# Kernel tuning notes

Hardware: AMD Instinct MI355X
Metric: run time of the kernel (lower is better)

The kernel has to match this reference:

```python
import jax, jax.numpy as jnp
import numpy as np

INPUT_DIM, HIDDEN, OUT_DIM = 7, 64, 4


def _lstm_layer(x_seq, W_ih, W_hh, b_ih, b_hh):
    """Single LSTM layer, batch_first x_seq [B,T,D] -> [B,T,H]. PyTorch gate order i,f,g,o."""
    B = x_seq.shape[0]
    H = W_hh.shape[1]
    # Precompute input projection for all timesteps (hoist GEMM out of the scan).
    x_proj = jnp.einsum('btd,gd->btg', x_seq, W_ih) + b_ih + b_hh  # [B,T,4H]

    def step(carry, xt):
        h, c = carry
        gates = xt + h @ W_hh.T  # [B,4H]
        i, f, g, o = jnp.split(gates, 4, axis=-1)
        i = jax.nn.sigmoid(i)
        f = jax.nn.sigmoid(f)
        g = jnp.tanh(g)
        o = jax.nn.sigmoid(o)
        c = f * c + i * g
        h = o * jnp.tanh(c)
        return (h, c), h

    h0 = jnp.zeros((B, H), x_seq.dtype)
    c0 = jnp.zeros((B, H), x_seq.dtype)
    (_, _), hs = jax.lax.scan(step, (h0, c0), jnp.swapaxes(x_proj, 0, 1))  # hs [T,B,H]
    return jnp.swapaxes(hs, 0, 1)  # [B,T,H]


def setup_inputs() -> dict:
    key = jax.random.key(0)
    ks = jax.random.split(key, 12)
    s = 0.1  # init scale ~ 1/sqrt(hidden)
    x = jax.random.normal(ks[0], (4096, 512, INPUT_DIM), dtype=jnp.float32)
    W_ih0 = jax.random.normal(ks[1], (4 * HIDDEN, INPUT_DIM), dtype=jnp.float32) * s
    W_hh0 = jax.random.normal(ks[2], (4 * HIDDEN, HIDDEN), dtype=jnp.float32) * s
    b_ih0 = jax.random.normal(ks[3], (4 * HIDDEN,), dtype=jnp.float32) * s
    b_hh0 = jax.random.normal(ks[4], (4 * HIDDEN,), dtype=jnp.float32) * s
    W_ih1 = jax.random.normal(ks[5], (4 * HIDDEN, HIDDEN), dtype=jnp.float32) * s
    W_hh1 = jax.random.normal(ks[6], (4 * HIDDEN, HIDDEN), dtype=jnp.float32) * s
    b_ih1 = jax.random.normal(ks[7], (4 * HIDDEN,), dtype=jnp.float32) * s
    b_hh1 = jax.random.normal(ks[8], (4 * HIDDEN,), dtype=jnp.float32) * s
    W_fc = jax.random.normal(ks[9], (OUT_DIM, HIDDEN), dtype=jnp.float32) * s
    b_fc = jax.random.normal(ks[10], (OUT_DIM,), dtype=jnp.float32) * s
    return {"x": x, "W_ih0": W_ih0, "W_hh0": W_hh0, "b_ih0": b_ih0, "b_hh0": b_hh0,
            "W_ih1": W_ih1, "W_hh1": W_hh1, "b_ih1": b_ih1, "b_hh1": b_hh1,
            "W_fc": W_fc, "b_fc": b_fc}


def reference(x, W_ih0, W_hh0, b_ih0, b_hh0, W_ih1, W_hh1, b_ih1, b_hh1, W_fc, b_fc):
    h1 = _lstm_layer(x, W_ih0, W_hh0, b_ih0, b_hh0)   # [B,T,H]
    h2 = _lstm_layer(h1, W_ih1, W_hh1, b_ih1, b_hh1)  # [B,T,H]
    last = h2[:, -1, :]                               # [B,H]
    return last @ W_fc.T + b_fc                       # [B,4]
```

## Files before the change

kernel.cpp:

```cpp
#include <hip/hip_runtime.h>

#define T_SEQ 512
#define HID 64
#define MB 16
#define NTHREADS 1024
#define A1STR 104
#define A2STR 104

typedef __attribute__((ext_vector_type(8))) short short8;
typedef __attribute__((ext_vector_type(4))) float floatx4;

#define LOG2E 1.4426950408889634f

__device__ __forceinline__ short f2bf_rne(float v) {
  unsigned u = __float_as_uint(v);
  return (short)((u + 0x7FFFu + ((u >> 16) & 1u)) >> 16);
}
__device__ __forceinline__ float rcp_(float x) { return __builtin_amdgcn_rcpf(x); }
__device__ __forceinline__ float exp2_(float x) { return __builtin_amdgcn_exp2f(x); }

__device__ __forceinline__ unsigned cvt_pk_bf16(float lo, float hi) {
  unsigned r;
  asm("v_cvt_pk_bf16_f32 %0, %1, %2" : "=v"(r) : "v"(lo), "v"(hi));
  return r;
}

__device__ __forceinline__ float gate_h(const floatx4 p, float& c) {
  float A = exp2_(-p[0]);
  float F = exp2_(-p[1]);
  float G = exp2_(p[2]);
  float O = exp2_(-p[3]);
  float t1 = (1.f + A) * (G + 1.f);
  float t2 = 1.f + F;
  float num = c * t1 + (G - 1.f) * t2;
  c = num * rcp_(t1 * t2);
  float C = exp2_((2.f * LOG2E) * c);
  return (C - 1.f) * rcp_((1.f + O) * (C + 1.f));
}

__device__ __forceinline__ int uofp(int p) {
  return (p & ~7) + ((p & 7) >> 1) + ((p & 1) << 2);
}

__device__ __forceinline__ short w1elem(int k, int n, float wsc,
                                        const float* __restrict__ Wih0,
                                        const float* __restrict__ Whh0) {
  float v;
  if      (k < 64) { v = Whh0[n*64 + uofp(k)]; }
  else if (k < 71) { v = Wih0[n*7 + (k - 64)]; }
  else return (short)0;
  return f2bf_rne(v * wsc);
}
__device__ __forceinline__ short w2elem(int k, int n, float wsc,
                                        const float* __restrict__ Wih1,
                                        const float* __restrict__ Whh1) {
  float v;
  if (k < 64) { v = Wih1[n*64 + uofp(k)]; }
  else        { v = Whh1[n*64 + uofp(k - 64)]; }
  return f2bf_rne(v * wsc);
}

#define MFMA(A, B, C) __builtin_amdgcn_mfma_f32_16x16x32_bf16((A), (B), (C), 0, 0, 0)

__global__ __launch_bounds__(NTHREADS, 4) void lstm_fused(
    const float* __restrict__ x,
    const float* __restrict__ Wih0, const float* __restrict__ Whh0,
    const float* __restrict__ bih0, const float* __restrict__ bhh0,
    const float* __restrict__ Wih1, const float* __restrict__ Whh1,
    const float* __restrict__ bih1, const float* __restrict__ bhh1,
    const float* __restrict__ Wfc,  const float* __restrict__ bfc,
    float* __restrict__ out)
{
  __shared__ __align__(16) short A1[2][MB][A1STR];
  __shared__ __align__(16) short A2[2][MB][A2STR];
  __shared__ float h2f[MB][HID + 4];

  const int tid  = threadIdx.x;
  const int lane = tid & 63;
  const int wave = tid >> 6;
  const int wl   = wave & 7;
  const bool isL1 = wave < 8;
  const int l15  = lane & 15;
  const int quad = lane >> 4;
  const int quad8= quad * 8;
  const int g4   = l15 & 3;
  const int b0   = blockIdx.x * MB;
  const int u0   = wl*8 + quad;
  const int u1   = u0 + 4;
  const int hpos = wl*8 + 2*quad;
  const int n0   = g4*64 + (wl*8 + (l15 >> 2));
  const int n1   = n0 + 4;
  const float wsc = (g4 == 2) ? 2.f * LOG2E : LOG2E;

  for (int i = tid; i < 2*MB*A1STR/2; i += NTHREADS) ((unsigned*)A1)[i] = 0u;
  for (int i = tid; i < 2*MB*A2STR/2; i += NTHREADS) ((unsigned*)A2)[i] = 0u;
  __syncthreads();

  const float* bi_ = isL1 ? bih0 : bih1;
  const float* bh_ = isL1 ? bhh0 : bhh1;
  floatx4 bia, bib;
  #pragma unroll
  for (int g = 0; g < 4; ++g) {
    float ws = (g == 2) ? 2.f * LOG2E : LOG2E;
    bia[g] = (bi_[g*64 + u0] + bh_[g*64 + u0]) * ws;
    bib[g] = (bi_[g*64 + u1] + bh_[g*64 + u1]) * ws;
  }

  const int xd2  = lane & 31;
  const int xrow = 2*wl + (lane >> 5);
  const bool xact = isL1 && (xd2 < 4);
  const float* xbase = x + ((size_t)(b0 + xrow) * T_SEQ) * 7 + 2*xd2;
  float xc0 = 0.f, xc1 = 0.f;
  if (xact) {
    *(unsigned*)&A1[0][xrow][64 + 2*xd2] =
        cvt_pk_bf16(xbase[0], (xd2 < 3) ? xbase[1] : 0.f);
    xc0 = xbase[7];
    xc1 = (xd2 < 3) ? xbase[8] : 0.f;
  }

  short8 WA[4], WB[4];
  if (isL1) {
    #pragma unroll
    for (int ks = 0; ks < 3; ++ks) {
      short8 fa, fb;
      #pragma unroll
      for (int jj = 0; jj < 8; ++jj) {
        fa[jj] = w1elem(ks*32 + quad8 + jj, n0, wsc, Wih0, Whh0);
        fb[jj] = w1elem(ks*32 + quad8 + jj, n1, wsc, Wih0, Whh0);
      }
      WA[ks] = fa; WB[ks] = fb;
    }
  } else {
    #pragma unroll
    for (int ks = 0; ks < 4; ++ks) {
      short8 fa, fb;
      #pragma unroll
      for (int jj = 0; jj < 8; ++jj) {
        fa[jj] = w2elem(ks*32 + quad8 + jj, n0, wsc, Wih1, Whh1);
        fb[jj] = w2elem(ks*32 + quad8 + jj, n1, wsc, Wih1, Whh1);
      }
      WA[ks] = fa; WB[ks] = fb;
    }
  }
  __syncthreads();

  float ca = 0.f, cb = 0.f;

#define STEP_X(NXT, XT)                                                      \
    if (xact) {                                                              \
      *(unsigned*)&A1[NXT][xrow][64 + 2*xd2] = cvt_pk_bf16(xc0, xc1);        \
      xc0 = xbase[7 * (XT)];                                                 \
      xc1 = (xd2 < 3) ? xbase[7 * (XT) + 1] : 0.f;                           \
    }

#define STEP_FULL(CUR, NXT, IT)                                              \
  {                                                                          \
    if (isL1) {                                                              \
      int xt_ = (IT) + 2; if (xt_ > T_SEQ - 1) xt_ = T_SEQ - 1;              \
      STEP_X(NXT, xt_)                                                       \
      short8 hf0 = *(const short8*)&A1[CUR][l15][     quad8];                \
      short8 hf1 = *(const short8*)&A1[CUR][l15][32 + quad8];                \
      short8 hfx = *(const short8*)&A1[CUR][l15][64 + quad8];                \
      floatx4 pa = bia, pb = bib;                                            \
      pa = MFMA(WA[0], hf0, pa);  pb = MFMA(WB[0], hf0, pb);                 \
      pa = MFMA(WA[1], hf1, pa);  pb = MFMA(WB[1], hf1, pb);                 \
      pa = MFMA(WA[2], hfx, pa);  pb = MFMA(WB[2], hfx, pb);                 \
      float ha = gate_h(pa, ca);                                             \
      float hb = gate_h(pb, cb);                                             \
      *(unsigned*)&A1[NXT][l15][hpos] = cvt_pk_bf16(ha, hb);                 \
    } else {                                                                 \
      short8 hf0 = *(const short8*)&A1[CUR][l15][     quad8];                \
      short8 hf1 = *(const short8*)&A1[CUR][l15][32 + quad8];                \
      short8 h20 = *(const short8*)&A2[CUR][l15][     quad8];                \
      short8 h21 = *(const short8*)&A2[CUR][l15][32 + quad8];                \
      floatx4 pa = bia, pb = bib;                                            \
      pa = MFMA(WA[0], hf0, pa);  pb = MFMA(WB[0], hf0, pb);                 \
      pa = MFMA(WA[1], hf1, pa);  pb = MFMA(WB[1], hf1, pb);                 \
      pa = MFMA(WA[2], h20, pa);  pb = MFMA(WB[2], h20, pb);                 \
      pa = MFMA(WA[3], h21, pa);  pb = MFMA(WB[3], h21, pb);                 \
      float ha = gate_h(pa, ca);                                             \
      float hb = gate_h(pb, cb);                                             \
      *(unsigned*)&A2[NXT][l15][hpos] = cvt_pk_bf16(ha, hb);                 \
    }                                                                        \
    __syncthreads();                                                         \
  }

  {
    if (isL1) {
      STEP_X(1, 2)
      short8 hf0 = *(const short8*)&A1[0][l15][     quad8];
      short8 hf1 = *(const short8*)&A1[0][l15][32 + quad8];
      short8 hfx = *(const short8*)&A1[0][l15][64 + quad8];
      floatx4 pa = bia, pb = bib;
      pa = MFMA(WA[0], hf0, pa);  pb = MFMA(WB[0], hf0, pb);
      pa = MFMA(WA[1], hf1, pa);  pb = MFMA(WB[1], hf1, pb);
      pa = MFMA(WA[2], hfx, pa);  pb = MFMA(WB[2], hfx, pb);
      float ha = gate_h(pa, ca);
      float hb = gate_h(pb, cb);
      *(unsigned*)&A1[1][l15][hpos] = cvt_pk_bf16(ha, hb);
    }
    __syncthreads();
  }

  #pragma unroll 1
  for (int k = 0; k < 255; ++k) {
    STEP_FULL(1, 0, 2*k + 1)
    STEP_FULL(0, 1, 2*k + 2)
  }
  STEP_FULL(1, 0, 511)

  {
    if (!isL1) {
      short8 hf0 = *(const short8*)&A1[0][l15][     quad8];
      short8 hf1 = *(const short8*)&A1[0][l15][32 + quad8];
      short8 h20 = *(const short8*)&A2[0][l15][     quad8];
      short8 h21 = *(const short8*)&A2[0][l15][32 + quad8];
      floatx4 pa = bia, pb = bib;
      pa = MFMA(WA[0], hf0, pa);  pb = MFMA(WB[0], hf0, pb);
      pa = MFMA(WA[1], hf1, pa);  pb = MFMA(WB[1], hf1, pb);
      pa = MFMA(WA[2], h20, pa);  pb = MFMA(WB[2], h20, pb);
      pa = MFMA(WA[3], h21, pa);  pb = MFMA(WB[3], h21, pb);
      h2f[l15][u0] = gate_h(pa, ca);
      h2f[l15][u1] = gate_h(pb, cb);
    }
    __syncthreads();
  }

  if (tid < MB * 4) {
    int bbf = tid >> 2, o = tid & 3;
    float acc = bfc[o];
    #pragma unroll 8
    for (int kk = 0; kk < HID; ++kk) acc += h2f[bbf][kk] * Wfc[o*HID + kk];
    out[(size_t)(b0 + bbf) * 4 + o] = acc;
  }
}

extern "C" void kernel_launch(void* const* d_in, const int* in_sizes, int n_in,
                              void* d_out, int out_size, void* d_ws, size_t ws_size,
                              hipStream_t stream) {
  const float* x    = (const float*)d_in[0];
  const float* Wih0 = (const float*)d_in[1];
  const float* Whh0 = (const float*)d_in[2];
  const float* bih0 = (const float*)d_in[3];
  const float* bhh0 = (const float*)d_in[4];
  const float* Wih1 = (const float*)d_in[5];
  const float* Whh1 = (const float*)d_in[6];
  const float* bih1 = (const float*)d_in[7];
  const float* bhh1 = (const float*)d_in[8];
  const float* Wfc  = (const float*)d_in[9];
  const float* bfc  = (const float*)d_in[10];
  (void)d_ws; (void)ws_size; (void)n_in; (void)out_size;

  const int B = in_sizes[0] / (T_SEQ * 7);
  dim3 grid(B / MB);
  lstm_fused<<<grid, NTHREADS, 0, stream>>>(x, Wih0, Whh0, bih0, bhh0,
                                            Wih1, Whh1, bih1, bhh1, Wfc, bfc,
                                            (float*)d_out);
}
```

Before: 427.4 us.

## Halve block to 8 waves with four gate tiles per wave and lighter barrier

Each block now uses 512 threads instead of 1024: 4 waves per LSTM layer, each computing four 16-column MFMA tiles and four gate cells per lane instead of two, with the weight fragments held in registers. This cuts the number of waves that meet at each per-timestep barrier and lets more independent MFMA chains overlap within a wave. The __syncthreads is also replaced by a raw LDS waitcnt plus s_barrier. In exchange, register pressure per thread doubles, the occupancy hint drops to 2, and there is less parallelism across waves inside each step.

Measured after the change: 426.3 us. About the same (-0.3%).

```diff
diff --git a/kernel.cpp b/kernel.cpp
--- a/kernel.cpp
+++ b/kernel.cpp
@@ -3,7 +3,7 @@
 #define T_SEQ 512
 #define HID 64
 #define MB 16
-#define NTHREADS 1024
+#define NTHREADS 512
 #define A1STR 104
 #define A2STR 104
 
@@ -23,6 +23,12 @@
   unsigned r;
   asm("v_cvt_pk_bf16_f32 %0, %1, %2" : "=v"(r) : "v"(lo), "v"(hi));
   return r;
+}
+
+__device__ __forceinline__ void barrier_lds() {
+  asm volatile("s_waitcnt lgkmcnt(0)" ::: "memory");
+  __builtin_amdgcn_s_barrier();
+  asm volatile("" ::: "memory");
 }
 
 __device__ __forceinline__ float gate_h(const floatx4 p, float& c) {
@@ -62,7 +68,7 @@
 
 #define MFMA(A, B, C) __builtin_amdgcn_mfma_f32_16x16x32_bf16((A), (B), (C), 0, 0, 0)
 
-__global__ __launch_bounds__(NTHREADS, 4) void lstm_fused(
+__global__ __launch_bounds__(NTHREADS, 2) void lstm_fused(
     const float* __restrict__ x,
     const float* __restrict__ Wih0, const float* __restrict__ Whh0,
     const float* __restrict__ bih0, const float* __restrict__ bhh0,
@@ -78,18 +84,16 @@
   const int tid  = threadIdx.x;
   const int lane = tid & 63;
   const int wave = tid >> 6;
-  const int wl   = wave & 7;
-  const bool isL1 = wave < 8;
+  const int w0   = wave & 3;
+  const bool isL1 = wave < 4;
   const int l15  = lane & 15;
   const int quad = lane >> 4;
   const int quad8= quad * 8;
   const int g4   = l15 & 3;
   const int b0   = blockIdx.x * MB;
-  const int u0   = wl*8 + quad;
-  const int u1   = u0 + 4;
-  const int hpos = wl*8 + 2*quad;
-  const int n0   = g4*64 + (wl*8 + (l15 >> 2));
-  const int n1   = n0 + 4;
+  const int ub   = w0*16 + quad;
+  const int hp0  = w0*16 + 2*quad;
+  const int hp1  = hp0 + 8;
   const float wsc = (g4 == 2) ? 2.f * LOG2E : LOG2E;
 
   for (int i = tid; i < 2*MB*A1STR/2; i += NTHREADS) ((unsigned*)A1)[i] = 0u;
@@ -98,16 +102,18 @@
 
   const float* bi_ = isL1 ? bih0 : bih1;
   const float* bh_ = isL1 ? bhh0 : bhh1;
-  floatx4 bia, bib;
+  floatx4 bs0, bs1, bs2, bs3;
   #pragma unroll
   for (int g = 0; g < 4; ++g) {
     float ws = (g == 2) ? 2.f * LOG2E : LOG2E;
-    bia[g] = (bi_[g*64 + u0] + bh_[g*64 + u0]) * ws;
-    bib[g] = (bi_[g*64 + u1] + bh_[g*64 + u1]) * ws;
-  }
-
-  const int xd2  = lane & 31;
-  const int xrow = 2*wl + (lane >> 5);
+    bs0[g] = (bi_[g*64 + ub     ] + bh_[g*64 + ub     ]) * ws;
+    bs1[g] = (bi_[g*64 + ub + 4 ] + bh_[g*64 + ub + 4 ]) * ws;
+    bs2[g] = (bi_[g*64 + ub + 8 ] + bh_[g*64 + ub + 8 ]) * ws;
+    bs3[g] = (bi_[g*64 + ub + 12] + bh_[g*64 + ub + 12]) * ws;
+  }
+
+  const int xd2  = l15;
+  const int xrow = 4*w0 + quad;
   const bool xact = isL1 && (xd2 < 4);
   const float* xbase = x + ((size_t)(b0 + xrow) * T_SEQ) * 7 + 2*xd2;
   float xc0 = 0.f, xc1 = 0.f;
@@ -118,33 +124,31 @@
     xc1 = (xd2 < 3) ? xbase[8] : 0.f;
   }
 
-  short8 WA[4], WB[4];
+  short8 W0[4], W1[4], W2[4], W3[4];
+#define LOADW1(Wt, t)                                                        \
+  { int nt = g4*64 + w0*16 + 4*(t) + (l15 >> 2);                             \
+    _Pragma("unroll")                                                        \
+    for (int ks = 0; ks < 3; ++ks) { short8 f;                               \
+      _Pragma("unroll")                                                      \
+      for (int jj = 0; jj < 8; ++jj)                                         \
+        f[jj] = w1elem(ks*32 + quad8 + jj, nt, wsc, Wih0, Whh0);             \
+      Wt[ks] = f; } }
+#define LOADW2(Wt, t)                                                        \
+  { int nt = g4*64 + w0*16 + 4*(t) + (l15 >> 2);                             \
+    _Pragma("unroll")                                                        \
+    for (int ks = 0; ks < 4; ++ks) { short8 f;                               \
+      _Pragma("unroll")                                                      \
+      for (int jj = 0; jj < 8; ++jj)                                         \
+        f[jj] = w2elem(ks*32 + quad8 + jj, nt, wsc, Wih1, Whh1);             \
+      Wt[ks] = f; } }
   if (isL1) {
-    #pragma unroll
-    for (int ks = 0; ks < 3; ++ks) {
-      short8 fa, fb;
-      #pragma unroll
-      for (int jj = 0; jj < 8; ++jj) {
-        fa[jj] = w1elem(ks*32 + quad8 + jj, n0, wsc, Wih0, Whh0);
-        fb[jj] = w1elem(ks*32 + quad8 + jj, n1, wsc, Wih0, Whh0);
-      }
-      WA[ks] = fa; WB[ks] = fb;
-    }
+    LOADW1(W0, 0) LOADW1(W1, 1) LOADW1(W2, 2) LOADW1(W3, 3)
   } else {
-    #pragma unroll
-    for (int ks = 0; ks < 4; ++ks) {
-      short8 fa, fb;
-      #pragma unroll
-      for (int jj = 0; jj < 8; ++jj) {
-        fa[jj] = w2elem(ks*32 + quad8 + jj, n0, wsc, Wih1, Whh1);
-        fb[jj] = w2elem(ks*32 + quad8 + jj, n1, wsc, Wih1, Whh1);
-      }
-      WA[ks] = fa; WB[ks] = fb;
-    }
+    LOADW2(W0, 0) LOADW2(W1, 1) LOADW2(W2, 2) LOADW2(W3, 3)
   }
   __syncthreads();
 
-  float ca = 0.f, cb = 0.f;
+  float c0 = 0.f, c1 = 0.f, c2 = 0.f, c3 = 0.f;
 
 #define STEP_X(NXT, XT)                                                      \
     if (xact) {                                                              \
@@ -152,6 +156,36 @@
       xc0 = xbase[7 * (XT)];                                                 \
       xc1 = (xd2 < 3) ? xbase[7 * (XT) + 1] : 0.f;                           \
     }
+
+#define L1_MFMAS                                                             \
+      floatx4 p0 = MFMA(W0[0], hf0, bs0);                                    \
+      floatx4 p1 = MFMA(W1[0], hf0, bs1);                                    \
+      floatx4 p2 = MFMA(W2[0], hf0, bs2);                                    \
+      floatx4 p3 = MFMA(W3[0], hf0, bs3);                                    \
+      p0 = MFMA(W0[1], hf1, p0);  p1 = MFMA(W1[1], hf1, p1);                 \
+      p2 = MFMA(W2[1], hf1, p2);  p3 = MFMA(W3[1], hf1, p3);                 \
+      p0 = MFMA(W0[2], hfx, p0);  p1 = MFMA(W1[2], hfx, p1);                 \
+      p2 = MFMA(W2[2], hfx, p2);  p3 = MFMA(W3[2], hfx, p3);
+
+#define L2_MFMAS                                                             \
+      floatx4 p0 = MFMA(W0[0], hf0, bs0);                                    \
+      floatx4 p1 = MFMA(W1[0], hf0, bs1);                                    \
+      floatx4 p2 = MFMA(W2[0], hf0, bs2);                                    \
+      floatx4 p3 = MFMA(W3[0], hf0, bs3);                                    \
+      p0 = MFMA(W0[1], hf1, p0);  p1 = MFMA(W1[1], hf1, p1);                 \
+      p2 = MFMA(W2[1], hf1, p2);  p3 = MFMA(W3[1], hf1, p3);                 \
+      p0 = MFMA(W0[2], h20, p0);  p1 = MFMA(W1[2], h20, p1);                 \
+      p2 = MFMA(W2[2], h20, p2);  p3 = MFMA(W3[2], h20, p3);                 \
+      p0 = MFMA(W0[3], h21, p0);  p1 = MFMA(W1[3], h21, p1);                 \
+      p2 = MFMA(W2[3], h21, p2);  p3 = MFMA(W3[3], h21, p3);
+
+#define GATES_AND_WRITE(DST)                                                 \
+      float h0 = gate_h(p0, c0);                                             \
+      float h1 = gate_h(p1, c1);                                             \
+      float h2 = gate_h(p2, c2);                                             \
+      float h3 = gate_h(p3, c3);                                             \
+      *(unsigned*)&DST[l15][hp0] = cvt_pk_bf16(h0, h1);                      \
+      *(unsigned*)&DST[l15][hp1] = cvt_pk_bf16(h2, h3);
 
 #define STEP_FULL(CUR, NXT, IT)                                              \
   {                                                                          \
@@ -161,28 +195,17 @@
       short8 hf0 = *(const short8*)&A1[CUR][l15][     quad8];                \
       short8 hf1 = *(const short8*)&A1[CUR][l15][32 + quad8];                \
       short8 hfx = *(const short8*)&A1[CUR][l15][64 + quad8];                \
-      floatx4 pa = bia, pb = bib;                                            \
-      pa = MFMA(WA[0], hf0, pa);  pb = MFMA(WB[0], hf0, pb);                 \
-      pa = MFMA(WA[1], hf1, pa);  pb = MFMA(WB[1], hf1, pb);                 \
-      pa = MFMA(WA[2], hfx, pa);  pb = MFMA(WB[2], hfx, pb);                 \
-      float ha = gate_h(pa, ca);                                             \
-      float hb = gate_h(pb, cb);                                             \
-      *(unsigned*)&A1[NXT][l15][hpos] = cvt_pk_bf16(ha, hb);                 \
+      L1_MFMAS                                                               \
+      GATES_AND_WRITE(A1[NXT])                                               \
     } else {                                                                 \
       short8 hf0 = *(const short8*)&A1[CUR][l15][     quad8];                \
       short8 hf1 = *(const short8*)&A1[CUR][l15][32 + quad8];                \
       short8 h20 = *(const short8*)&A2[CUR][l15][     quad8];                \
       short8 h21 = *(const short8*)&A2[CUR][l15][32 + quad8];                \
-      floatx4 pa = bia, pb = bib;                                            \
-      pa = MFMA(WA[0], hf0, pa);  pb = MFMA(WB[0], hf0, pb);                 \
-      pa = MFMA(WA[1], hf1, pa);  pb = MFMA(WB[1], hf1, pb);                 \
-      pa = MFMA(WA[2], h20, pa);  pb = MFMA(WB[2], h20, pb);                 \
-      pa = MFMA(WA[3], h21, pa);  pb = MFMA(WB[3], h21, pb);                 \
-      float ha = gate_h(pa, ca);                                             \
-      float hb = gate_h(pb, cb);                                             \
-      *(unsigned*)&A2[NXT][l15][hpos] = cvt_pk_bf16(ha, hb);                 \
+      L2_MFMAS                                                               \
+      GATES_AND_WRITE(A2[NXT])                                               \
     }                                                                        \
-    __syncthreads();                                                         \
+    barrier_lds();                                                           \
   }
 
   {
@@ -191,15 +214,10 @@
       short8 hf0 = *(const short8*)&A1[0][l15][     quad8];
       short8 hf1 = *(const short8*)&A1[0][l15][32 + quad8];
       short8 hfx = *(const short8*)&A1[0][l15][64 + quad8];
-      floatx4 pa = bia, pb = bib;
-      pa = MFMA(WA[0], hf0, pa);  pb = MFMA(WB[0], hf0, pb);
-      pa = MFMA(WA[1], hf1, pa);  pb = MFMA(WB[1], hf1, pb);
-      pa = MFMA(WA[2], hfx, pa);  pb = MFMA(WB[2], hfx, pb);
-      float ha = gate_h(pa, ca);
-      float hb = gate_h(pb, cb);
-      *(unsigned*)&A1[1][l15][hpos] = cvt_pk_bf16(ha, hb);
+      L1_MFMAS
+      GATES_AND_WRITE(A1[1])
     }
-    __syncthreads();
+    barrier_lds();
   }
 
   #pragma unroll 1
@@ -215,13 +233,11 @@
       short8 hf1 = *(const short8*)&A1[0][l15][32 + quad8];
       short8 h20 = *(const short8*)&A2[0][l15][     quad8];
       short8 h21 = *(const short8*)&A2[0][l15][32 + quad8];
-      floatx4 pa = bia, pb = bib;
-      pa = MFMA(WA[0], hf0, pa);  pb = MFMA(WB[0], hf0, pb);
-      pa = MFMA(WA[1], hf1, pa);  pb = MFMA(WB[1], hf1, pb);
-      pa = MFMA(WA[2], h20, pa);  pb = MFMA(WB[2], h20, pb);
-      pa = MFMA(WA[3], h21, pa);  pb = MFMA(WB[3], h21, pb);
-      h2f[l15][u0] = gate_h(pa, ca);
-      h2f[l15][u1] = gate_h(pb, cb);
+      L2_MFMAS
+      h2f[l15][ub     ] = gate_h(p0, c0);
+      h2f[l15][ub + 4 ] = gate_h(p1, c1);
+      h2f[l15][ub + 8 ] = gate_h(p2, c2);
+      h2f[l15][ub + 12] = gate_h(p3, c3);
     }
     __syncthreads();
   }
```

## Merge layer-1 and layer-2 LSTM work into each wave with 512-thread blocks

Applied to the files above, without the earlier changes.

Before, 16 waves per block were split by layer: eight waves ran layer 1 and eight ran layer 2. Now each of 8 waves computes its hidden-unit slice for both layers in every step. All MFMAs are issued together and a sched_barrier separates them from the gate math. A custom barrier (waitcnt lgkmcnt(0) plus s_barrier) replaces __syncthreads. The goal is to overlap the two layers' MFMA and transcendental latency inside one wave and make each barrier cheaper, at the cost of more registers per thread (both weight sets) and half the waves per block.

New measurement: 441.1 us. +3.2%, slower.

```diff
diff --git a/kernel.cpp b/kernel.cpp
--- a/kernel.cpp
+++ b/kernel.cpp
@@ -3,7 +3,7 @@
 #define T_SEQ 512
 #define HID 64
 #define MB 16
-#define NTHREADS 1024
+#define NTHREADS 512
 #define A1STR 104
 #define A2STR 104
 
@@ -23,6 +23,12 @@
   unsigned r;
   asm("v_cvt_pk_bf16_f32 %0, %1, %2" : "=v"(r) : "v"(lo), "v"(hi));
   return r;
+}
+
+__device__ __forceinline__ void barrier_lds() {
+  asm volatile("s_waitcnt lgkmcnt(0)" ::: "memory");
+  __builtin_amdgcn_s_barrier();
+  asm volatile("" ::: "memory");
 }
 
 __device__ __forceinline__ float gate_h(const floatx4 p, float& c) {
@@ -62,7 +68,7 @@
 
 #define MFMA(A, B, C) __builtin_amdgcn_mfma_f32_16x16x32_bf16((A), (B), (C), 0, 0, 0)
 
-__global__ __launch_bounds__(NTHREADS, 4) void lstm_fused(
+__global__ __launch_bounds__(NTHREADS, 2) void lstm_fused(
     const float* __restrict__ x,
     const float* __restrict__ Wih0, const float* __restrict__ Whh0,
     const float* __restrict__ bih0, const float* __restrict__ bhh0,
@@ -78,37 +84,34 @@
   const int tid  = threadIdx.x;
   const int lane = tid & 63;
   const int wave = tid >> 6;
-  const int wl   = wave & 7;
-  const bool isL1 = wave < 8;
   const int l15  = lane & 15;
   const int quad = lane >> 4;
   const int quad8= quad * 8;
   const int g4   = l15 & 3;
   const int b0   = blockIdx.x * MB;
-  const int u0   = wl*8 + quad;
-  const int u1   = u0 + 4;
-  const int hpos = wl*8 + 2*quad;
-  const int n0   = g4*64 + (wl*8 + (l15 >> 2));
-  const int n1   = n0 + 4;
+  const int ua   = wave*8 + quad;
+  const int hpos = wave*8 + 2*quad;
+  const int na   = g4*64 + wave*8 + (l15 >> 2);
+  const int nb   = na + 4;
   const float wsc = (g4 == 2) ? 2.f * LOG2E : LOG2E;
 
   for (int i = tid; i < 2*MB*A1STR/2; i += NTHREADS) ((unsigned*)A1)[i] = 0u;
   for (int i = tid; i < 2*MB*A2STR/2; i += NTHREADS) ((unsigned*)A2)[i] = 0u;
   __syncthreads();
 
-  const float* bi_ = isL1 ? bih0 : bih1;
-  const float* bh_ = isL1 ? bhh0 : bhh1;
-  floatx4 bia, bib;
+  floatx4 b1a, b1b, b2a, b2b;
   #pragma unroll
   for (int g = 0; g < 4; ++g) {
     float ws = (g == 2) ? 2.f * LOG2E : LOG2E;
-    bia[g] = (bi_[g*64 + u0] + bh_[g*64 + u0]) * ws;
-    bib[g] = (bi_[g*64 + u1] + bh_[g*64 + u1]) * ws;
+    b1a[g] = (bih0[g*64 + ua    ] + bhh0[g*64 + ua    ]) * ws;
+    b1b[g] = (bih0[g*64 + ua + 4] + bhh0[g*64 + ua + 4]) * ws;
+    b2a[g] = (bih1[g*64 + ua    ] + bhh1[g*64 + ua    ]) * ws;
+    b2b[g] = (bih1[g*64 + ua + 4] + bhh1[g*64 + ua + 4]) * ws;
   }
 
   const int xd2  = lane & 31;
-  const int xrow = 2*wl + (lane >> 5);
-  const bool xact = isL1 && (xd2 < 4);
+  const int xrow = 2*wave + (lane >> 5);
+  const bool xact = (xd2 < 4);
   const float* xbase = x + ((size_t)(b0 + xrow) * T_SEQ) * 7 + 2*xd2;
   float xc0 = 0.f, xc1 = 0.f;
   if (xact) {
@@ -118,33 +121,30 @@
     xc1 = (xd2 < 3) ? xbase[8] : 0.f;
   }
 
-  short8 WA[4], WB[4];
-  if (isL1) {
+  short8 W1a[3], W1b[3], W2a[4], W2b[4];
+  #pragma unroll
+  for (int ks = 0; ks < 3; ++ks) {
+    short8 fa, fb;
     #pragma unroll
-    for (int ks = 0; ks < 3; ++ks) {
-      short8 fa, fb;
-      #pragma unroll
-      for (int jj = 0; jj < 8; ++jj) {
-        fa[jj] = w1elem(ks*32 + quad8 + jj, n0, wsc, Wih0, Whh0);
-        fb[jj] = w1elem(ks*32 + quad8 + jj, n1, wsc, Wih0, Whh0);
-      }
-      WA[ks] = fa; WB[ks] = fb;
+    for (int jj = 0; jj < 8; ++jj) {
+      fa[jj] = w1elem(ks*32 + quad8 + jj, na, wsc, Wih0, Whh0);
+      fb[jj] = w1elem(ks*32 + quad8 + jj, nb, wsc, Wih0, Whh0);
     }
-  } else {
+    W1a[ks] = fa; W1b[ks] = fb;
+  }
+  #pragma unroll
+  for (int ks = 0; ks < 4; ++ks) {
+    short8 fa, fb;
     #pragma unroll
-    for (int ks = 0; ks < 4; ++ks) {
-      short8 fa, fb;
-      #pragma unroll
-      for (int jj = 0; jj < 8; ++jj) {
-        fa[jj] = w2elem(ks*32 + quad8 + jj, n0, wsc, Wih1, Whh1);
-        fb[jj] = w2elem(ks*32 + quad8 + jj, n1, wsc, Wih1, Whh1);
-      }
-      WA[ks] = fa; WB[ks] = fb;
+    for (int jj = 0; jj < 8; ++jj) {
+      fa[jj] = w2elem(ks*32 + quad8 + jj, na, wsc, Wih1, Whh1);
+      fb[jj] = w2elem(ks*32 + quad8 + jj, nb, wsc, Wih1, Whh1);
     }
+    W2a[ks] = fa; W2b[ks] = fb;
   }
   __syncthreads();
 
-  float ca = 0.f, cb = 0.f;
+  float c1a = 0.f, c1b = 0.f, c2a = 0.f, c2b = 0.f;
 
 #define STEP_X(NXT, XT)                                                      \
     if (xact) {                                                              \
@@ -155,51 +155,45 @@
 
 #define STEP_FULL(CUR, NXT, IT)                                              \
   {                                                                          \
-    if (isL1) {                                                              \
-      int xt_ = (IT) + 2; if (xt_ > T_SEQ - 1) xt_ = T_SEQ - 1;              \
-      STEP_X(NXT, xt_)                                                       \
-      short8 hf0 = *(const short8*)&A1[CUR][l15][     quad8];                \
-      short8 hf1 = *(const short8*)&A1[CUR][l15][32 + quad8];                \
-      short8 hfx = *(const short8*)&A1[CUR][l15][64 + quad8];                \
-      floatx4 pa = bia, pb = bib;                                            \
-      pa = MFMA(WA[0], hf0, pa);  pb = MFMA(WB[0], hf0, pb);                 \
-      pa = MFMA(WA[1], hf1, pa);  pb = MFMA(WB[1], hf1, pb);                 \
-      pa = MFMA(WA[2], hfx, pa);  pb = MFMA(WB[2], hfx, pb);                 \
-      float ha = gate_h(pa, ca);                                             \
-      float hb = gate_h(pb, cb);                                             \
-      *(unsigned*)&A1[NXT][l15][hpos] = cvt_pk_bf16(ha, hb);                 \
-    } else {                                                                 \
-      short8 hf0 = *(const short8*)&A1[CUR][l15][     quad8];                \
-      short8 hf1 = *(const short8*)&A1[CUR][l15][32 + quad8];                \
-      short8 h20 = *(const short8*)&A2[CUR][l15][     quad8];                \
-      short8 h21 = *(const short8*)&A2[CUR][l15][32 + quad8];                \
-      floatx4 pa = bia, pb = bib;                                            \
-      pa = MFMA(WA[0], hf0, pa);  pb = MFMA(WB[0], hf0, pb);                 \
-      pa = MFMA(WA[1], hf1, pa);  pb = MFMA(WB[1], hf1, pb);                 \
-      pa = MFMA(WA[2], h20, pa);  pb = MFMA(WB[2], h20, pb);                 \
-      pa = MFMA(WA[3], h21, pa);  pb = MFMA(WB[3], h21, pb);                 \
-      float ha = gate_h(pa, ca);                                             \
-      float hb = gate_h(pb, cb);                                             \
-      *(unsigned*)&A2[NXT][l15][hpos] = cvt_pk_bf16(ha, hb);                 \
-    }                                                                        \
-    __syncthreads();                                                         \
+    short8 hf0 = *(const short8*)&A1[CUR][l15][     quad8];                  \
+    short8 hf1 = *(const short8*)&A1[CUR][l15][32 + quad8];                  \
+    short8 hfx = *(const short8*)&A1[CUR][l15][64 + quad8];                  \
+    short8 h20 = *(const short8*)&A2[CUR][l15][     quad8];                  \
+    short8 h21 = *(const short8*)&A2[CUR][l15][32 + quad8];                  \
+    floatx4 p1a = MFMA(W1a[0], hf0, b1a);                                    \
+    floatx4 p1b = MFMA(W1b[0], hf0, b1b);                                    \
+    p1a = MFMA(W1a[1], hf1, p1a);  p1b = MFMA(W1b[1], hf1, p1b);             \
+    p1a = MFMA(W1a[2], hfx, p1a);  p1b = MFMA(W1b[2], hfx, p1b);             \
+    floatx4 p2a = MFMA(W2a[0], hf0, b2a);                                    \
+    floatx4 p2b = MFMA(W2b[0], hf0, b2b);                                    \
+    p2a = MFMA(W2a[1], hf1, p2a);  p2b = MFMA(W2b[1], hf1, p2b);             \
+    p2a = MFMA(W2a[2], h20, p2a);  p2b = MFMA(W2b[2], h20, p2b);             \
+    p2a = MFMA(W2a[3], h21, p2a);  p2b = MFMA(W2b[3], h21, p2b);             \
+    __builtin_amdgcn_sched_barrier(0);                                       \
+    int xt_ = (IT) + 2; if (xt_ > T_SEQ - 1) xt_ = T_SEQ - 1;                \
+    STEP_X(NXT, xt_)                                                         \
+    float h1a = gate_h(p1a, c1a);                                            \
+    float h1b = gate_h(p1b, c1b);                                            \
+    *(unsigned*)&A1[NXT][l15][hpos] = cvt_pk_bf16(h1a, h1b);                 \
+    float h2a = gate_h(p2a, c2a);                                            \
+    float h2b = gate_h(p2b, c2b);                                            \
+    *(unsigned*)&A2[NXT][l15][hpos] = cvt_pk_bf16(h2a, h2b);                 \
+    barrier_lds();                                                           \
   }
 
   {
-    if (isL1) {
-      STEP_X(1, 2)
-      short8 hf0 = *(const short8*)&A1[0][l15][     quad8];
-      short8 hf1 = *(const short8*)&A1[0][l15][32 + quad8];
-      short8 hfx = *(const short8*)&A1[0][l15][64 + quad8];
-      floatx4 pa = bia, pb = bib;
-      pa = MFMA(WA[0], hf0, pa);  pb = MFMA(WB[0], hf0, pb);
-      pa = MFMA(WA[1], hf1, pa);  pb = MFMA(WB[1], hf1, pb);
-      pa = MFMA(WA[2], hfx, pa);  pb = MFMA(WB[2], hfx, pb);
-      float ha = gate_h(pa, ca);
-      float hb = gate_h(pb, cb);
-      *(unsigned*)&A1[1][l15][hpos] = cvt_pk_bf16(ha, hb);
-    }
-    __syncthreads();
+    short8 hf0 = *(const short8*)&A1[0][l15][     quad8];
+    short8 hf1 = *(const short8*)&A1[0][l15][32 + quad8];
+    short8 hfx = *(const short8*)&A1[0][l15][64 + quad8];
+    floatx4 p1a = MFMA(W1a[0], hf0, b1a);
+    floatx4 p1b = MFMA(W1b[0], hf0, b1b);
+    p1a = MFMA(W1a[1], hf1, p1a);  p1b = MFMA(W1b[1], hf1, p1b);
+    p1a = MFMA(W1a[2], hfx, p1a);  p1b = MFMA(W1b[2], hfx, p1b);
+    STEP_X(1, 2)
+    float h1a = gate_h(p1a, c1a);
+    float h1b = gate_h(p1b, c1b);
+    *(unsigned*)&A1[1][l15][hpos] = cvt_pk_bf16(h1a, h1b);
+    barrier_lds();
   }
 
   #pragma unroll 1
@@ -210,19 +204,17 @@
   STEP_FULL(1, 0, 511)
 
   {
-    if (!isL1) {
-      short8 hf0 = *(const short8*)&A1[0][l15][     quad8];
-      short8 hf1 = *(const short8*)&A1[0][l15][32 + quad8];
-      short8 h20 = *(const short8*)&A2[0][l15][     quad8];
-      short8 h21 = *(const short8*)&A2[0][l15][32 + quad8];
-      floatx4 pa = bia, pb = bib;
-      pa = MFMA(WA[0], hf0, pa);  pb = MFMA(WB[0], hf0, pb);
-      pa = MFMA(WA[1], hf1, pa);  pb = MFMA(WB[1], hf1, pb);
-      pa = MFMA(WA[2], h20, pa);  pb = MFMA(WB[2], h20, pb);
-      pa = MFMA(WA[3], h21, pa);  pb = MFMA(WB[3], h21, pb);
-      h2f[l15][u0] = gate_h(pa, ca);
-      h2f[l15][u1] = gate_h(pb, cb);
-    }
+    short8 hf0 = *(const short8*)&A1[0][l15][     quad8];
+    short8 hf1 = *(const short8*)&A1[0][l15][32 + quad8];
+    short8 h20 = *(const short8*)&A2[0][l15][     quad8];
+    short8 h21 = *(const short8*)&A2[0][l15][32 + quad8];
+    floatx4 p2a = MFMA(W2a[0], hf0, b2a);
+    floatx4 p2b = MFMA(W2b[0], hf0, b2b);
+    p2a = MFMA(W2a[1], hf1, p2a);  p2b = MFMA(W2b[1], hf1, p2b);
+    p2a = MFMA(W2a[2], h20, p2a);  p2b = MFMA(W2b[2], h20, p2b);
+    p2a = MFMA(W2a[3], h21, p2a);  p2b = MFMA(W2b[3], h21, p2b);
+    h2f[l15][ua    ] = gate_h(p2a, c2a);
+    h2f[l15][ua + 4] = gate_h(p2b, c2b);
     __syncthreads();
   }
 
```
